# Kernel optimization log

Hardware: AMD Instinct MI355X
Metric: run time of the kernel (lower is better)

Reference implementation:

```python
import jax, jax.numpy as jnp
import numpy as np

B = 2048
F = 267          # frame_size
L = 32           # latent_size
H = 256          # hidden_size (hard-coded in module)
E = 8            # num_experts
G = 64           # gate hidden size (hard-coded)
IN0 = L + F      # decoder layer0 input (latent + frame*cond_frames)
IN1 = L + H      # decoder inter input
OUT = F          # num_future_predictions * frame_size


def _lin_init(key, out_dim, in_dim):
    # kaiming-uniform-like scale
    bound = float(np.sqrt(1.0 / in_dim))
    return jax.random.uniform(key, (out_dim, in_dim), jnp.float32, -bound, bound)


def setup_inputs() -> dict:
    key = jax.random.key(0)
    ks = jax.random.split(key, 24)
    d = {}
    d["x"] = jax.random.normal(ks[0], (B, F), jnp.float32)
    d["c"] = jax.random.normal(ks[1], (B, F), jnp.float32)
    # encoder
    d["fc1_w"] = _lin_init(ks[2], H, 2 * F); d["fc1_b"] = jnp.zeros((H,), jnp.float32)
    d["fc2_w"] = _lin_init(ks[3], H, F + H); d["fc2_b"] = jnp.zeros((H,), jnp.float32)
    d["mu_w"] = _lin_init(ks[4], L, F + H);  d["mu_b"] = jnp.zeros((L,), jnp.float32)
    d["lv_w"] = _lin_init(ks[5], L, F + H);  d["lv_b"] = jnp.zeros((L,), jnp.float32)
    # gate
    d["g0_w"] = _lin_init(ks[6], G, IN0); d["g0_b"] = jnp.zeros((G,), jnp.float32)
    d["g1_w"] = _lin_init(ks[7], G, G);   d["g1_b"] = jnp.zeros((G,), jnp.float32)
    d["g2_w"] = _lin_init(ks[8], E, G);   d["g2_b"] = jnp.zeros((E,), jnp.float32)
    # expert weights [E, in, out], biases [E, out], bias filled 0.01 as in module
    d["w0"] = jax.random.uniform(ks[9], (E, IN0, H), jnp.float32, -1, 1) * np.sqrt(1.0 / IN0)
    d["b0"] = jnp.full((E, H), 0.01, jnp.float32)
    d["w1"] = jax.random.uniform(ks[10], (E, IN1, H), jnp.float32, -1, 1) * np.sqrt(1.0 / IN1)
    d["b1"] = jnp.full((E, H), 0.01, jnp.float32)
    d["w2"] = jax.random.uniform(ks[11], (E, IN1, OUT), jnp.float32, -1, 1) * np.sqrt(1.0 / IN1)
    d["b2"] = jnp.full((E, OUT), 0.01, jnp.float32)
    return d


def reference(x, c, fc1_w, fc1_b, fc2_w, fc2_b, mu_w, mu_b, lv_w, lv_b,
              g0_w, g0_b, g1_w, g1_b, g2_w, g2_b, w0, b0, w1, b1, w2, b2):
    elu = jax.nn.elu
    # ---- encoder ----
    h1 = elu(jnp.concatenate([x, c], axis=1) @ fc1_w.T + fc1_b)
    h2 = elu(jnp.concatenate([x, h1], axis=1) @ fc2_w.T + fc2_b)
    s = jnp.concatenate([x, h2], axis=1)
    mu = s @ mu_w.T + mu_b
    logvar = s @ lv_w.T + lv_b
    eps = jax.random.normal(jax.random.key(42), mu.shape, mu.dtype)
    z = mu + eps * jnp.exp(0.5 * logvar)
    # ---- mixed decoder ----
    g = elu(jnp.concatenate([z, c], axis=1) @ g0_w.T + g0_b)
    g = elu(g @ g1_w.T + g1_b)
    coeff = jax.nn.softmax(g @ g2_w.T + g2_b, axis=1)  # [B, E]
    layer_out = c
    for (W, bvec, act) in ((w0, b0, True), (w1, b1, True), (w2, b2, False)):
        inp = jnp.concatenate([z, layer_out], axis=1)          # [B, in]
        # per-expert GEMM then coefficient mixing (same math as per-sample
        # mixed-weight bmm: coeff @ flat_weight then baddbmm)
        out = jnp.einsum('be,bi,eio->bo', coeff, inp, W, optimize=True)
        out = out + coeff @ bvec                               # mixed bias
        layer_out = elu(out) if act else out
    return (layer_out, mu, logvar)
```

## Files before the change

kernel.cpp:

```cpp
#include <hip/hip_runtime.h>
#include <math.h>
#include <stdint.h>

#define DI __device__ __forceinline__

typedef __attribute__((ext_vector_type(8))) short bf16x8;
typedef __attribute__((ext_vector_type(4))) float f32x4;
typedef __attribute__((ext_vector_type(4))) int i32x4;

#define MFMA16(av, bv, acc) __builtin_amdgcn_mfma_f32_16x16x32_bf16(av, bv, acc, 0, 0, 0)

DI float elu_f(float v) { return v > 0.f ? v : expm1f(v); }

DI unsigned short f2bf(float f) {
  uint32_t u = __float_as_uint(f);
  return (unsigned short)((u + 0x7FFFu + ((u >> 16) & 1u)) >> 16);
}

DI void threefry2x32(uint32_t k0, uint32_t k1, uint32_t& x0, uint32_t& x1) {
  uint32_t ks0 = k0, ks1 = k1, ks2 = k0 ^ k1 ^ 0x1BD11BDAu;
  x0 += ks0; x1 += ks1;
#define TFR(r) { x0 += x1; x1 = (x1 << r) | (x1 >> (32 - r)); x1 ^= x0; }
  TFR(13) TFR(15) TFR(26) TFR(6)   x0 += ks1; x1 += ks2 + 1u;
  TFR(17) TFR(29) TFR(16) TFR(24)  x0 += ks2; x1 += ks0 + 2u;
  TFR(13) TFR(15) TFR(26) TFR(6)   x0 += ks0; x1 += ks1 + 3u;
  TFR(17) TFR(29) TFR(16) TFR(24)  x0 += ks1; x1 += ks2 + 4u;
  TFR(13) TFR(15) TFR(26) TFR(6)   x0 += ks2; x1 += ks0 + 5u;
#undef TFR
}

DI float erfinv_f(float x) {
  float w = -logf((1.0f - x) * (1.0f + x));
  float p;
  if (w < 5.0f) {
    w -= 2.5f;
    p = 2.81022636e-08f;
    p = fmaf(p, w, 3.43273939e-07f);
    p = fmaf(p, w, -3.5233877e-06f);
    p = fmaf(p, w, -4.39150654e-06f);
    p = fmaf(p, w, 0.00021858087f);
    p = fmaf(p, w, -0.00125372503f);
    p = fmaf(p, w, -0.00417768164f);
    p = fmaf(p, w, 0.246640727f);
    p = fmaf(p, w, 1.50140941f);
  } else {
    w = sqrtf(w) - 3.0f;
    p = -0.000200214257f;
    p = fmaf(p, w, 0.000100950558f);
    p = fmaf(p, w, 0.00134934322f);
    p = fmaf(p, w, -0.00367342844f);
    p = fmaf(p, w, 0.00573950773f);
    p = fmaf(p, w, -0.0076224613f);
    p = fmaf(p, w, 0.00943887047f);
    p = fmaf(p, w, 1.00167406f);
    p = fmaf(p, w, 2.83297682f);
  }
  return p * x;
}

struct MegaArgs {
  const float *x, *c;
  const float *fc1w, *fc1b, *fc2w, *fc2b, *muw, *mub, *lvw, *lvb;
  const float *g0w, *g0b, *g1w, *g1b, *g2w, *g2b;
  const float *w0, *b0, *w1, *b1, *w2, *b2;
  unsigned short *Ax, *Axh, *A0, *A1, *A2;
  unsigned short *fc1t, *fc2t, *mlvt, *g0t, *g1t, *w0b, *w1b, *w2b;
  float *cf, *outY, *outMu, *outLv;
};

template <int KT, int NE, int D, bool ELU, bool OUTF32>
__global__ __launch_bounds__(128, 2)
void pipe32(const unsigned short* __restrict__ A,
            const unsigned short* __restrict__ Wt, int N,
            const float* __restrict__ bias,
            const float* __restrict__ cfp,
            unsigned short* __restrict__ Cb, int ldcb, int cb_off,
            float* __restrict__ Cf) {
  constexpr int Kp = KT * 32, TT = NE * KT;
  __shared__ float bias_s[NE * 32];
  __shared__ float cfs[(NE > 1) ? 256 : 1];
  const int tid = threadIdx.x, lane = tid & 63, wv = tid >> 6;
  const int q = lane >> 4, l16 = lane & 15;
  const int m0 = blockIdx.x * 32;
  const int n0 = blockIdx.y * 32 + wv * 16;
  const int gc = n0 + l16;
  const int wrow = (gc < N) ? gc : (N - 1);
  const unsigned short* wlane = Wt + (size_t)wrow * Kp + q * 8;

  bf16x8 ring[D];
#pragma unroll
  for (int g = 0; g < D; g++) {
    if (g < TT) {
      int e = g / KT, c = g % KT;
      ring[g] = *(const bf16x8*)(wlane + (size_t)e * N * Kp + c * 32);
    }
  }
  bf16x8 areg[2][KT];
#pragma unroll
  for (int t = 0; t < 2; t++) {
    const unsigned short* alane = A + (size_t)(m0 + t * 16 + l16) * Kp + q * 8;
#pragma unroll
    for (int c = 0; c < KT; c++) areg[t][c] = *(const bf16x8*)(alane + c * 32);
  }

  if (NE == 1) {
    if (tid < 32) {
      int col = blockIdx.y * 32 + tid;
      bias_s[tid] = (col < N) ? bias[col] : 0.f;
    }
  } else {
    for (int idx = tid; idx < NE * 32; idx += 128) {
      int e = idx >> 5, col = blockIdx.y * 32 + (idx & 31);
      bias_s[idx] = (col < N) ? bias[(size_t)e * N + col] : 0.f;
    }
    for (int idx = tid; idx < 256; idx += 128)
      cfs[idx] = cfp[(size_t)(m0 + (idx >> 3)) * 8 + (idx & 7)];
  }
  __syncthreads();

  f32x4 acc[2] = {{0.f, 0.f, 0.f, 0.f}, {0.f, 0.f, 0.f, 0.f}};
  f32x4 accF[2] = {{0.f, 0.f, 0.f, 0.f}, {0.f, 0.f, 0.f, 0.f}};
#pragma unroll
  for (int g = 0; g < TT; g++) {
    const int e = g / KT, c = g % KT;
    bf16x8 bv = ring[g % D];
    acc[0] = MFMA16(areg[0][c], bv, acc[0]);
    acc[1] = MFMA16(areg[1][c], bv, acc[1]);
    if (g + D < TT) {
      int e2 = (g + D) / KT, c2 = (g + D) % KT;
      ring[g % D] = *(const bf16x8*)(wlane + (size_t)e2 * N * Kp + c2 * 32);
    }
    if (NE > 1 && c == KT - 1) {
      float bv2 = bias_s[e * 32 + wv * 16 + l16];
#pragma unroll
      for (int t = 0; t < 2; t++)
#pragma unroll
        for (int r = 0; r < 4; r++) {
          float ce = cfs[(t * 16 + q * 4 + r) * 8 + e];
          accF[t][r] += ce * (acc[t][r] + bv2);
          acc[t][r] = 0.f;
        }
    }
  }

  if (gc < N) {
#pragma unroll
    for (int t = 0; t < 2; t++)
#pragma unroll
      for (int r = 0; r < 4; r++) {
        int row = m0 + t * 16 + q * 4 + r;
        float v = (NE > 1) ? accF[t][r] : (acc[t][r] + bias_s[wv * 16 + l16]);
        if (ELU) v = elu_f(v);
        if (OUTF32) Cf[(size_t)row * 267 + gc] = v;
        else Cb[(size_t)row * ldcb + cb_off + gc] = f2bf(v);
      }
  }
}

DI void transpose_params(int t, const MegaArgs& a, const float*& W,
                         unsigned short*& D, int& K, int& N2, int& Kp2,
                         int& ldW, int& e, int& kt, int& nt) {
  if (t < 160)      { e = t / 20;  int lt = t % 20;  kt = lt / 4; nt = lt % 4; W = a.w0; D = a.w0b; K = 299; N2 = 256; Kp2 = 320; ldW = 256; }
  else if (t < 320) { int u = t - 160; e = u / 20; int lt = u % 20; kt = lt / 4; nt = lt % 4; W = a.w1; D = a.w1b; K = 288; N2 = 256; Kp2 = 288; ldW = 256; }
  else              { int u = t - 320; e = u / 25; int lt = u % 25; kt = lt / 5; nt = lt % 5; W = a.w2; D = a.w2b; K = 288; N2 = 267; Kp2 = 288; ldW = 267; }
}

DI void transpose128(unsigned short (*T)[72], int t, const MegaArgs& a) {
  const int tid = threadIdx.x;
  const float* W; unsigned short* D; int K, N2, Kp2, ldW, e, kt, nt;
  transpose_params(t, a, W, D, K, N2, Kp2, ldW, e, kt, nt);
  const int k0 = kt * 64, n0 = nt * 64;
  const float* We = W + (size_t)e * K * ldW;
  const int jj = tid & 63, ii0 = tid >> 6;
#pragma unroll
  for (int p = 0; p < 32; p++) {
    int i = ii0 + p * 2;
    int gk = k0 + i, gn = n0 + jj;
    float v = (gk < K && gn < N2) ? We[(size_t)gk * ldW + gn] : 0.f;
    T[jj][i] = f2bf(v);
  }
  __syncthreads();
  const int j0 = tid >> 2, chb = tid & 3;
#pragma unroll
  for (int jh = 0; jh < 2; jh++) {
    int j = j0 + jh * 32;
    int gn = n0 + j;
    if (gn < N2) {
      unsigned short* drow = D + ((size_t)e * N2 + gn) * Kp2 + k0;
#pragma unroll
      for (int s = 0; s < 2; s++) {
        int ch = chb + s * 4;
        if (k0 + ch * 8 < Kp2) {
          i32x4 v = *(i32x4*)(&T[j][ch * 8]);
          *(i32x4*)(drow + ch * 8) = v;
        }
      }
    }
  }
}

DI void transpose256(unsigned short (*T)[72], int t, const MegaArgs& a) {
  const int tid = threadIdx.x;
  const float* W; unsigned short* D; int K, N2, Kp2, ldW, e, kt, nt;
  transpose_params(t, a, W, D, K, N2, Kp2, ldW, e, kt, nt);
  const int k0 = kt * 64, n0 = nt * 64;
  const float* We = W + (size_t)e * K * ldW;
  const int jj = tid & 63, ii0 = tid >> 6;
#pragma unroll
  for (int p = 0; p < 16; p++) {
    int i = ii0 + p * 4;
    int gk = k0 + i, gn = n0 + jj;
    float v = (gk < K && gn < N2) ? We[(size_t)gk * ldW + gn] : 0.f;
    T[jj][i] = f2bf(v);
  }
  __syncthreads();
  int j = tid >> 2, chb = tid & 3;
  int gn = n0 + j;
  if (gn < N2) {
    unsigned short* drow = D + ((size_t)e * N2 + gn) * Kp2 + k0;
#pragma unroll
    for (int s = 0; s < 2; s++) {
      int ch = chb + s * 4;
      if (k0 + ch * 8 < Kp2) {
        i32x4 v = *(i32x4*)(&T[j][ch * 8]);
        *(i32x4*)(drow + ch * 8) = v;
      }
    }
  }
}

DI void conv128(const float* src, unsigned short* dst, int Ks, int Kp2) {
  for (int k = threadIdx.x; k < Kp2; k += 128)
    dst[k] = (k < Ks) ? f2bf(src[k]) : (unsigned short)0;
}

__global__ __launch_bounds__(256) void k_prep0(MegaArgs a) {
  const int bb = blockIdx.x, tid = threadIdx.x;
  if (bb < 512) {
    for (int rr = 0; rr < 4; rr++) {
      int b = bb * 4 + rr;
      const float* xr = a.x + (size_t)b * 267;
      const float* cr = a.c + (size_t)b * 267;
      unsigned short* axr = a.Ax + (size_t)b * 544;
      for (int k = tid; k < 544; k += 256) {
        float v = (k < 267) ? xr[k] : ((k < 534) ? cr[k - 267] : 0.f);
        axr[k] = f2bf(v);
      }
      unsigned short* ahr = a.Axh + (size_t)b * 544;
      for (int k = tid; k < 267; k += 256) ahr[k] = f2bf(xr[k]);
      for (int k = 523 + tid; k < 544; k += 256) ahr[k] = 0;
      unsigned short* a0r = a.A0 + (size_t)b * 320;
      for (int k = tid; k < 288; k += 256)
        a0r[32 + k] = (k < 267) ? f2bf(cr[k]) : (unsigned short)0;
    }
  } else {
    int r = bb - 512;
    const float* src = a.fc1w + (size_t)r * 534;
    unsigned short* dst = a.fc1t + (size_t)r * 544;
    for (int k = tid; k < 544; k += 256)
      dst[k] = (k < 534) ? f2bf(src[k]) : (unsigned short)0;
  }
}

__global__ __launch_bounds__(128, 2) void k_fc1mix(MegaArgs a) {
  __shared__ float bias_s[32];
  __shared__ __align__(16) unsigned short T[64][72];
  const int bid = blockIdx.x, tid = threadIdx.x;
  if (bid < 512) {
    const int lane = tid & 63, wv = tid >> 6;
    const int q = lane >> 4, l16 = lane & 15;
    const int bx = bid & 63, by = bid >> 6;
    const int m0 = bx * 32;
    const int gc = by * 32 + wv * 16 + l16;
    const unsigned short* wlane = a.fc1t + (size_t)gc * 544 + q * 8;

    bf16x8 ring[12];
#pragma unroll
    for (int g = 0; g < 12; g++)
      ring[g] = *(const bf16x8*)(wlane + g * 32);
    bf16x8 areg[2][17];
#pragma unroll
    for (int t = 0; t < 2; t++) {
      const unsigned short* alane = a.Ax + (size_t)(m0 + t * 16 + l16) * 544 + q * 8;
#pragma unroll
      for (int c = 0; c < 17; c++) areg[t][c] = *(const bf16x8*)(alane + c * 32);
    }
    if (tid < 32) bias_s[tid] = a.fc1b[by * 32 + tid];
    __syncthreads();

    f32x4 acc[2] = {{0.f, 0.f, 0.f, 0.f}, {0.f, 0.f, 0.f, 0.f}};
#pragma unroll
    for (int g = 0; g < 17; g++) {
      bf16x8 bv = ring[g % 12];
      acc[0] = MFMA16(areg[0][g], bv, acc[0]);
      acc[1] = MFMA16(areg[1][g], bv, acc[1]);
      if (g + 12 < 17)
        ring[g % 12] = *(const bf16x8*)(wlane + (g + 12) * 32);
    }
    float bc = bias_s[wv * 16 + l16];
#pragma unroll
    for (int t = 0; t < 2; t++)
#pragma unroll
      for (int r = 0; r < 4; r++) {
        int row = m0 + t * 16 + q * 4 + r;
        a.Axh[(size_t)row * 544 + 267 + gc] = f2bf(elu_f(acc[t][r] + bc));
      }
  } else if (bid < 897) {
    int c = bid - 512;
    if (c < 256)      conv128(a.fc2w + (size_t)c * 523, a.fc2t + (size_t)c * 544, 523, 544);
    else if (c < 320) { int n = c - 256;
                        conv128((n < 32) ? (a.muw + (size_t)n * 523) : (a.lvw + (size_t)(n - 32) * 523),
                                a.mlvt + (size_t)n * 544, 523, 544); }
    else if (c < 384) { int n = c - 320;
                        conv128(a.g0w + (size_t)n * 299, a.g0t + (size_t)n * 320, 299, 320); }
    else              conv128(a.g1w, a.g1t, 4096, 4096);
  } else {
    transpose128(T, bid - 897, a);
  }
}

__global__ __launch_bounds__(256) void k_enc(MegaArgs a) {
  __shared__ __align__(16) unsigned short sA[16][552];
  __shared__ float mlvS[16 * 65];
  __shared__ __align__(16) unsigned short A0p[16 * 328];
  __shared__ __align__(16) unsigned short gaB[16 * 72];
  __shared__ __align__(16) unsigned short g1B[64 * 72];
  __shared__ float g2wT[64 * 8];
  __shared__ float gB[16 * 65];
  __shared__ float lg[16 * 8];
  __shared__ __align__(16) unsigned short T[64][72];

  const int bid = blockIdx.x;
  if (bid >= 128) { transpose256(T, 160 + (bid - 128), a); return; }

  const int tid = threadIdx.x, lane = tid & 63, wid = tid >> 6;
  const int q = lane >> 4, l16 = lane & 15;
  const int m0 = bid * 16;

  for (int idx = tid; idx < 16 * 68; idx += 256) {
    int row = idx / 68, ch = idx % 68;
    *(i32x4*)(&sA[row][ch * 8]) =
        *(const i32x4*)(a.Axh + (size_t)(m0 + row) * 544 + ch * 8);
  }
  bf16x8 areg[17];
  {
    const unsigned short* alane = a.Axh + (size_t)(m0 + l16) * 544 + q * 8;
#pragma unroll
    for (int c = 0; c < 17; c++) areg[c] = *(const bf16x8*)(alane + c * 32);
  }
  for (int idx = tid; idx < 512; idx += 256)
    g2wT[(idx & 63) * 8 + (idx >> 6)] = a.g2w[idx];
  __syncthreads();

#pragma unroll
  for (int i = 0; i < 4; i++) {
    const int col = (wid * 4 + i) * 16 + l16;
    const unsigned short* wl = a.fc2t + (size_t)col * 544 + q * 8;
    bf16x8 ring[8];
#pragma unroll
    for (int g = 0; g < 8; g++) ring[g] = *(const bf16x8*)(wl + g * 32);
    f32x4 acc = {0.f, 0.f, 0.f, 0.f};
#pragma unroll
    for (int g = 0; g < 17; g++) {
      acc = MFMA16(areg[g], ring[g % 8], acc);
      if (g + 8 < 17) ring[g % 8] = *(const bf16x8*)(wl + (g + 8) * 32);
    }
    float bc = a.fc2b[col];
#pragma unroll
    for (int r = 0; r < 4; r++)
      sA[q * 4 + r][267 + col] = f2bf(elu_f(acc[r] + bc));
  }
  __syncthreads();

  const int cl = wid * 16 + l16;
  {
    const unsigned short* wlA = a.mlvt + (size_t)cl * 544 + q * 8;
    bf16x8 ring[8];
#pragma unroll
    for (int g = 0; g < 8; g++) ring[g] = *(const bf16x8*)(wlA + g * 32);
    f32x4 acc = {0.f, 0.f, 0.f, 0.f};
#pragma unroll
    for (int g = 0; g < 17; g++) {
      bf16x8 av = *(const bf16x8*)(&sA[l16][g * 32 + q * 8]);
      acc = MFMA16(av, ring[g % 8], acc);
      if (g + 8 < 17) ring[g % 8] = *(const bf16x8*)(wlA + (g + 8) * 32);
    }
#pragma unroll
    for (int r = 0; r < 4; r++) mlvS[(q * 4 + r) * 65 + cl] = acc[r];
  }
  for (int idx = tid; idx < 576; idx += 256) {
    int row = idx / 36, ch = 4 + idx % 36;
    *(i32x4*)(A0p + row * 328 + ch * 8) =
        *(const i32x4*)(a.A0 + (size_t)(m0 + row) * 320 + ch * 8);
  }
  if (tid < 16) { i32x4 z4 = {0, 0, 0, 0}; *(i32x4*)(A0p + tid * 328 + 320) = z4; }
  for (int idx = tid; idx < 512; idx += 256) {
    int row = idx >> 3, ch = idx & 7;
    *(i32x4*)(g1B + row * 72 + ch * 8) = *(const i32x4*)(a.g1t + (size_t)row * 64 + ch * 8);
  }
  __syncthreads();

  {
    const int m = tid >> 4, j0 = (tid & 15) * 2, R = m0 + m;
#pragma unroll
    for (int jj = 0; jj < 2; jj++) {
      int j = j0 + jj;
      float mu = mlvS[m * 65 + j] + a.mub[j];
      float lvv = mlvS[m * 65 + j + 32] + a.lvb[j];
      uint32_t x0 = 0u, x1 = (uint32_t)(R * 32 + j);
      threefry2x32(0u, 42u, x0, x1);
      uint32_t bits = x0 ^ x1;
      float f = __uint_as_float((bits >> 9) | 0x3F800000u) - 1.0f;
      const float lo = -0.99999994039535522461f;
      float u = fmaf(f, 2.0f, lo);
      u = fmaxf(u, lo);
      float eps = 1.41421356237f * erfinv_f(u);
      float z = fmaf(eps, expf(0.5f * lvv), mu);
      a.outMu[(size_t)R * 32 + j] = mu;
      a.outLv[(size_t)R * 32 + j] = lvv;
      unsigned short zb = f2bf(z);
      A0p[m * 328 + j] = zb;
      a.A0[(size_t)R * 320 + j] = zb;
      a.A1[(size_t)R * 288 + j] = zb;
      a.A2[(size_t)R * 288 + j] = zb;
    }
  }
  __syncthreads();

  {
    const unsigned short* wlC = a.g0t + (size_t)cl * 320 + q * 8;
    bf16x8 ring2[8];
#pragma unroll
    for (int g = 0; g < 8; g++) ring2[g] = *(const bf16x8*)(wlC + g * 32);
    f32x4 accC = {0.f, 0.f, 0.f, 0.f};
#pragma unroll
    for (int g = 0; g < 10; g++) {
      bf16x8 av = *(const bf16x8*)(A0p + l16 * 328 + g * 32 + q * 8);
      accC = MFMA16(av, ring2[g % 8], accC);
      if (g + 8 < 10) ring2[g % 8] = *(const bf16x8*)(wlC + (g + 8) * 32);
    }
    float bc = a.g0b[cl];
#pragma unroll
    for (int r = 0; r < 4; r++)
      gaB[(q * 4 + r) * 72 + cl] = f2bf(elu_f(accC[r] + bc));
  }
  __syncthreads();

  {
    f32x4 accD = {0.f, 0.f, 0.f, 0.f};
#pragma unroll
    for (int tau = 0; tau < 2; tau++) {
      bf16x8 av = *(const bf16x8*)(gaB + l16 * 72 + tau * 32 + q * 8);
      bf16x8 bv = *(const bf16x8*)(g1B + cl * 72 + tau * 32 + q * 8);
      accD = MFMA16(av, bv, accD);
    }
    float bc = a.g1b[cl];
#pragma unroll
    for (int r = 0; r < 4; r++)
      gB[(q * 4 + r) * 65 + cl] = elu_f(accD[r] + bc);
  }
  __syncthreads();

  if (tid < 128) {
    int r = tid >> 3, e = tid & 7;
    float d = a.g2b[e];
#pragma unroll 8
    for (int k = 0; k < 64; k++) d = fmaf(gB[r * 65 + k], g2wT[k * 8 + e], d);
    lg[r * 8 + e] = d;
  }
  __syncthreads();
  if (tid < 16) {
    float mx = lg[tid * 8];
#pragma unroll
    for (int e2 = 1; e2 < 8; e2++) mx = fmaxf(mx, lg[tid * 8 + e2]);
    float s = 0.f, ex[8];
#pragma unroll
    for (int e2 = 0; e2 < 8; e2++) { ex[e2] = expf(lg[tid * 8 + e2] - mx); s += ex[e2]; }
    float inv = 1.f / s;
#pragma unroll
    for (int e2 = 0; e2 < 8; e2++) a.cf[(size_t)(m0 + tid) * 8 + e2] = ex[e2] * inv;
  }
}

extern "C" void kernel_launch(void* const* d_in, const int* in_sizes, int n_in,
                              void* d_out, int out_size, void* d_ws, size_t ws_size,
                              hipStream_t stream) {
  (void)in_sizes; (void)n_in; (void)out_size; (void)ws_size;
  float* out = (float*)d_out;
  float* ws = (float*)d_ws;

  MegaArgs a;
  a.x    = (const float*)d_in[0];
  a.c    = (const float*)d_in[1];
  a.fc1w = (const float*)d_in[2];  a.fc1b = (const float*)d_in[3];
  a.fc2w = (const float*)d_in[4];  a.fc2b = (const float*)d_in[5];
  a.muw  = (const float*)d_in[6];  a.mub  = (const float*)d_in[7];
  a.lvw  = (const float*)d_in[8];  a.lvb  = (const float*)d_in[9];
  a.g0w  = (const float*)d_in[10]; a.g0b  = (const float*)d_in[11];
  a.g1w  = (const float*)d_in[12]; a.g1b  = (const float*)d_in[13];
  a.g2w  = (const float*)d_in[14]; a.g2b  = (const float*)d_in[15];
  a.w0   = (const float*)d_in[16]; a.b0   = (const float*)d_in[17];
  a.w1   = (const float*)d_in[18]; a.b1   = (const float*)d_in[19];
  a.w2   = (const float*)d_in[20]; a.b2   = (const float*)d_in[21];

  a.outY  = out;
  a.outMu = out + 2048 * 267;
  a.outLv = a.outMu + 2048 * 32;

  a.Ax   = (unsigned short*)(ws);
  a.Axh  = (unsigned short*)(ws + 557056);
  a.A0   = (unsigned short*)(ws + 1671168);
  a.A1   = (unsigned short*)(ws + 1998848);
  a.A2   = (unsigned short*)(ws + 2293760);
  a.fc1t = (unsigned short*)(ws + 2588672);
  a.fc2t = (unsigned short*)(ws + 2658304);
  a.mlvt = (unsigned short*)(ws + 2727936);
  a.g0t  = (unsigned short*)(ws + 2745344);
  a.g1t  = (unsigned short*)(ws + 2755584);
  a.w0b  = (unsigned short*)(ws + 2757632);
  a.w1b  = (unsigned short*)(ws + 3085312);
  a.w2b  = (unsigned short*)(ws + 3380224);
  a.cf   = ws + 3687808;

  k_prep0<<<768, 256, 0, stream>>>(a);
  k_fc1mix<<<1057, 128, 0, stream>>>(a);
  k_enc<<<488, 256, 0, stream>>>(a);
  pipe32<10, 8, 12, true, false><<<dim3(64, 8), 128, 0, stream>>>(
      a.A0, a.w0b, 256, a.b0, a.cf, a.A1, 288, 32, nullptr);
  pipe32<9, 8, 12, true, false><<<dim3(64, 8), 128, 0, stream>>>(
      a.A1, a.w1b, 256, a.b1, a.cf, a.A2, 288, 32, nullptr);
  pipe32<9, 8, 12, false, true><<<dim3(64, 9), 128, 0, stream>>>(
      a.A2, a.w2b, 267, a.b2, a.cf, nullptr, 0, 0, a.outY);
}
```

Baseline: 189.5 us.

## Split encoder fc2 into its own wide-grid kernel before mu/logvar and gate

The fused encoder kernel that ran fc2, mu/logvar and the gate MLP on 16-row tiles over 128 blocks is split in two. fc2 now runs as a separate 512-block kernel with 32x32 output tiles, writing its ELU output into a second bf16 buffer. A smaller kernel then does mu/logvar, sampling and the gate. The aim is to raise parallelism for the fc2 GEMM, which previously ran on only 128 blocks, at the cost of an extra launch and a round trip of the hidden activations through global memory.

```diff
diff --git a/kernel.cpp b/kernel.cpp
--- a/kernel.cpp
+++ b/kernel.cpp
@@ -63,7 +63,7 @@
   const float *fc1w, *fc1b, *fc2w, *fc2b, *muw, *mub, *lvw, *lvb;
   const float *g0w, *g0b, *g1w, *g1b, *g2w, *g2b;
   const float *w0, *b0, *w1, *b1, *w2, *b2;
-  unsigned short *Ax, *Axh, *A0, *A1, *A2;
+  unsigned short *Ax, *Axh, *Axh2, *A0, *A1, *A2;
   unsigned short *fc1t, *fc2t, *mlvt, *g0t, *g1t, *w0b, *w1b, *w2b;
   float *cf, *outY, *outMu, *outLv;
 };
@@ -199,36 +199,6 @@
   }
 }
 
-DI void transpose256(unsigned short (*T)[72], int t, const MegaArgs& a) {
-  const int tid = threadIdx.x;
-  const float* W; unsigned short* D; int K, N2, Kp2, ldW, e, kt, nt;
-  transpose_params(t, a, W, D, K, N2, Kp2, ldW, e, kt, nt);
-  const int k0 = kt * 64, n0 = nt * 64;
-  const float* We = W + (size_t)e * K * ldW;
-  const int jj = tid & 63, ii0 = tid >> 6;
-#pragma unroll
-  for (int p = 0; p < 16; p++) {
-    int i = ii0 + p * 4;
-    int gk = k0 + i, gn = n0 + jj;
-    float v = (gk < K && gn < N2) ? We[(size_t)gk * ldW + gn] : 0.f;
-    T[jj][i] = f2bf(v);
-  }
-  __syncthreads();
-  int j = tid >> 2, chb = tid & 3;
-  int gn = n0 + j;
-  if (gn < N2) {
-    unsigned short* drow = D + ((size_t)e * N2 + gn) * Kp2 + k0;
-#pragma unroll
-    for (int s = 0; s < 2; s++) {
-      int ch = chb + s * 4;
-      if (k0 + ch * 8 < Kp2) {
-        i32x4 v = *(i32x4*)(&T[j][ch * 8]);
-        *(i32x4*)(drow + ch * 8) = v;
-      }
-    }
-  }
-}
-
 DI void conv128(const float* src, unsigned short* dst, int Ks, int Kp2) {
   for (int k = threadIdx.x; k < Kp2; k += 128)
     dst[k] = (k < Ks) ? f2bf(src[k]) : (unsigned short)0;
@@ -247,8 +217,9 @@
         axr[k] = f2bf(v);
       }
       unsigned short* ahr = a.Axh + (size_t)b * 544;
-      for (int k = tid; k < 267; k += 256) ahr[k] = f2bf(xr[k]);
-      for (int k = 523 + tid; k < 544; k += 256) ahr[k] = 0;
+      unsigned short* ah2 = a.Axh2 + (size_t)b * 544;
+      for (int k = tid; k < 267; k += 256) { unsigned short v = f2bf(xr[k]); ahr[k] = v; ah2[k] = v; }
+      for (int k = 523 + tid; k < 544; k += 256) { ahr[k] = 0; ah2[k] = 0; }
       unsigned short* a0r = a.A0 + (size_t)b * 320;
       for (int k = tid; k < 288; k += 256)
         a0r[32 + k] = (k < 267) ? f2bf(cr[k]) : (unsigned short)0;
@@ -319,8 +290,55 @@
   }
 }
 
-__global__ __launch_bounds__(256) void k_enc(MegaArgs a) {
-  __shared__ __align__(16) unsigned short sA[16][552];
+__global__ __launch_bounds__(128, 2) void k_fc2mix(MegaArgs a) {
+  __shared__ float bias_s[32];
+  __shared__ __align__(16) unsigned short T[64][72];
+  const int bid = blockIdx.x, tid = threadIdx.x;
+  if (bid < 512) {
+    const int lane = tid & 63, wv = tid >> 6;
+    const int q = lane >> 4, l16 = lane & 15;
+    const int bx = bid & 63, by = bid >> 6;
+    const int m0 = bx * 32;
+    const int gc = by * 32 + wv * 16 + l16;
+    const unsigned short* wlane = a.fc2t + (size_t)gc * 544 + q * 8;
+
+    bf16x8 ring[12];
+#pragma unroll
+    for (int g = 0; g < 12; g++)
+      ring[g] = *(const bf16x8*)(wlane + g * 32);
+    bf16x8 areg[2][17];
+#pragma unroll
+    for (int t = 0; t < 2; t++) {
+      const unsigned short* alane = a.Axh + (size_t)(m0 + t * 16 + l16) * 544 + q * 8;
+#pragma unroll
+      for (int c = 0; c < 17; c++) areg[t][c] = *(const bf16x8*)(alane + c * 32);
+    }
+    if (tid < 32) bias_s[tid] = a.fc2b[by * 32 + tid];
+    __syncthreads();
+
+    f32x4 acc[2] = {{0.f, 0.f, 0.f, 0.f}, {0.f, 0.f, 0.f, 0.f}};
+#pragma unroll
+    for (int g = 0; g < 17; g++) {
+      bf16x8 bv = ring[g % 12];
+      acc[0] = MFMA16(areg[0][g], bv, acc[0]);
+      acc[1] = MFMA16(areg[1][g], bv, acc[1]);
+      if (g + 12 < 17)
+        ring[g % 12] = *(const bf16x8*)(wlane + (g + 12) * 32);
+    }
+    float bc = bias_s[wv * 16 + l16];
+#pragma unroll
+    for (int t = 0; t < 2; t++)
+#pragma unroll
+      for (int r = 0; r < 4; r++) {
+        int row = m0 + t * 16 + q * 4 + r;
+        a.Axh2[(size_t)row * 544 + 267 + gc] = f2bf(elu_f(acc[t][r] + bc));
+      }
+  } else {
+    transpose128(T, 160 + (bid - 512), a);
+  }
+}
+
+__global__ __launch_bounds__(256, 2) void k_mulv_gate(MegaArgs a) {
   __shared__ float mlvS[16 * 65];
   __shared__ __align__(16) unsigned short A0p[16 * 328];
   __shared__ __align__(16) unsigned short gaB[16 * 72];
@@ -328,66 +346,27 @@
   __shared__ float g2wT[64 * 8];
   __shared__ float gB[16 * 65];
   __shared__ float lg[16 * 8];
-  __shared__ __align__(16) unsigned short T[64][72];
-
-  const int bid = blockIdx.x;
-  if (bid >= 128) { transpose256(T, 160 + (bid - 128), a); return; }
-
   const int tid = threadIdx.x, lane = tid & 63, wid = tid >> 6;
   const int q = lane >> 4, l16 = lane & 15;
-  const int m0 = bid * 16;
-
-  for (int idx = tid; idx < 16 * 68; idx += 256) {
-    int row = idx / 68, ch = idx % 68;
-    *(i32x4*)(&sA[row][ch * 8]) =
-        *(const i32x4*)(a.Axh + (size_t)(m0 + row) * 544 + ch * 8);
-  }
+  const int m0 = blockIdx.x * 16;
+  const int cl = wid * 16 + l16;
+
+  const unsigned short* alane = a.Axh2 + (size_t)(m0 + l16) * 544 + q * 8;
+  const unsigned short* wlA = a.mlvt + (size_t)cl * 544 + q * 8;
+  bf16x8 ring[8];
+#pragma unroll
+  for (int g = 0; g < 8; g++) ring[g] = *(const bf16x8*)(wlA + g * 32);
   bf16x8 areg[17];
-  {
-    const unsigned short* alane = a.Axh + (size_t)(m0 + l16) * 544 + q * 8;
-#pragma unroll
-    for (int c = 0; c < 17; c++) areg[c] = *(const bf16x8*)(alane + c * 32);
-  }
-  for (int idx = tid; idx < 512; idx += 256)
-    g2wT[(idx & 63) * 8 + (idx >> 6)] = a.g2w[idx];
-  __syncthreads();
-
-#pragma unroll
-  for (int i = 0; i < 4; i++) {
-    const int col = (wid * 4 + i) * 16 + l16;
-    const unsigned short* wl = a.fc2t + (size_t)col * 544 + q * 8;
-    bf16x8 ring[8];
-#pragma unroll
-    for (int g = 0; g < 8; g++) ring[g] = *(const bf16x8*)(wl + g * 32);
-    f32x4 acc = {0.f, 0.f, 0.f, 0.f};
-#pragma unroll
-    for (int g = 0; g < 17; g++) {
-      acc = MFMA16(areg[g], ring[g % 8], acc);
-      if (g + 8 < 17) ring[g % 8] = *(const bf16x8*)(wl + (g + 8) * 32);
-    }
-    float bc = a.fc2b[col];
-#pragma unroll
-    for (int r = 0; r < 4; r++)
-      sA[q * 4 + r][267 + col] = f2bf(elu_f(acc[r] + bc));
-  }
-  __syncthreads();
-
-  const int cl = wid * 16 + l16;
-  {
-    const unsigned short* wlA = a.mlvt + (size_t)cl * 544 + q * 8;
-    bf16x8 ring[8];
-#pragma unroll
-    for (int g = 0; g < 8; g++) ring[g] = *(const bf16x8*)(wlA + g * 32);
-    f32x4 acc = {0.f, 0.f, 0.f, 0.f};
-#pragma unroll
-    for (int g = 0; g < 17; g++) {
-      bf16x8 av = *(const bf16x8*)(&sA[l16][g * 32 + q * 8]);
-      acc = MFMA16(av, ring[g % 8], acc);
-      if (g + 8 < 17) ring[g % 8] = *(const bf16x8*)(wlA + (g + 8) * 32);
-    }
-#pragma unroll
-    for (int r = 0; r < 4; r++) mlvS[(q * 4 + r) * 65 + cl] = acc[r];
-  }
+#pragma unroll
+  for (int c = 0; c < 17; c++) areg[c] = *(const bf16x8*)(alane + c * 32);
+  f32x4 acc = {0.f, 0.f, 0.f, 0.f};
+#pragma unroll
+  for (int g = 0; g < 17; g++) {
+    acc = MFMA16(areg[g], ring[g % 8], acc);
+    if (g + 8 < 17) ring[g % 8] = *(const bf16x8*)(wlA + (g + 8) * 32);
+  }
+#pragma unroll
+  for (int r = 0; r < 4; r++) mlvS[(q * 4 + r) * 65 + cl] = acc[r];
   for (int idx = tid; idx < 576; idx += 256) {
     int row = idx / 36, ch = 4 + idx % 36;
     *(i32x4*)(A0p + row * 328 + ch * 8) =
@@ -398,6 +377,8 @@
     int row = idx >> 3, ch = idx & 7;
     *(i32x4*)(g1B + row * 72 + ch * 8) = *(const i32x4*)(a.g1t + (size_t)row * 64 + ch * 8);
   }
+  for (int idx = tid; idx < 512; idx += 256)
+    g2wT[(idx & 63) * 8 + (idx >> 6)] = a.g2w[idx];
   __syncthreads();
 
   {
@@ -427,18 +408,18 @@
   }
   __syncthreads();
 
+  const unsigned short* wlC = a.g0t + (size_t)cl * 320 + q * 8;
+  bf16x8 ring2[8];
+#pragma unroll
+  for (int g = 0; g < 8; g++) ring2[g] = *(const bf16x8*)(wlC + g * 32);
+  f32x4 accC = {0.f, 0.f, 0.f, 0.f};
+#pragma unroll
+  for (int g = 0; g < 10; g++) {
+    bf16x8 av = *(const bf16x8*)(A0p + l16 * 328 + g * 32 + q * 8);
+    accC = MFMA16(av, ring2[g % 8], accC);
+    if (g + 8 < 10) ring2[g % 8] = *(const bf16x8*)(wlC + (g + 8) * 32);
+  }
   {
-    const unsigned short* wlC = a.g0t + (size_t)cl * 320 + q * 8;
-    bf16x8 ring2[8];
-#pragma unroll
-    for (int g = 0; g < 8; g++) ring2[g] = *(const bf16x8*)(wlC + g * 32);
-    f32x4 accC = {0.f, 0.f, 0.f, 0.f};
-#pragma unroll
-    for (int g = 0; g < 10; g++) {
-      bf16x8 av = *(const bf16x8*)(A0p + l16 * 328 + g * 32 + q * 8);
-      accC = MFMA16(av, ring2[g % 8], accC);
-      if (g + 8 < 10) ring2[g % 8] = *(const bf16x8*)(wlC + (g + 8) * 32);
-    }
     float bc = a.g0b[cl];
 #pragma unroll
     for (int r = 0; r < 4; r++)
@@ -446,14 +427,14 @@
   }
   __syncthreads();
 
+  f32x4 accD = {0.f, 0.f, 0.f, 0.f};
+#pragma unroll
+  for (int tau = 0; tau < 2; tau++) {
+    bf16x8 av = *(const bf16x8*)(gaB + l16 * 72 + tau * 32 + q * 8);
+    bf16x8 bv = *(const bf16x8*)(g1B + cl * 72 + tau * 32 + q * 8);
+    accD = MFMA16(av, bv, accD);
+  }
   {
-    f32x4 accD = {0.f, 0.f, 0.f, 0.f};
-#pragma unroll
-    for (int tau = 0; tau < 2; tau++) {
-      bf16x8 av = *(const bf16x8*)(gaB + l16 * 72 + tau * 32 + q * 8);
-      bf16x8 bv = *(const bf16x8*)(g1B + cl * 72 + tau * 32 + q * 8);
-      accD = MFMA16(av, bv, accD);
-    }
     float bc = a.g1b[cl];
 #pragma unroll
     for (int r = 0; r < 4; r++)
@@ -509,6 +490,7 @@
 
   a.Ax   = (unsigned short*)(ws);
   a.Axh  = (unsigned short*)(ws + 557056);
+  a.Axh2 = (unsigned short*)(ws + 1114112);
   a.A0   = (unsigned short*)(ws + 1671168);
   a.A1   = (unsigned short*)(ws + 1998848);
   a.A2   = (unsigned short*)(ws + 2293760);
@@ -524,7 +506,8 @@
 
   k_prep0<<<768, 256, 0, stream>>>(a);
   k_fc1mix<<<1057, 128, 0, stream>>>(a);
-  k_enc<<<488, 256, 0, stream>>>(a);
+  k_fc2mix<<<872, 128, 0, stream>>>(a);
+  k_mulv_gate<<<128, 256, 0, stream>>>(a);
   pipe32<10, 8, 12, true, false><<<dim3(64, 8), 128, 0, stream>>>(
       a.A0, a.w0b, 256, a.b0, a.cf, a.A1, 288, 32, nullptr);
   pipe32<9, 8, 12, true, false><<<dim3(64, 8), 128, 0, stream>>>(
```

After: 191.9 us. Within noise of the previous version (+1.2%).
